# Optimization experiments

Hardware: AMD Instinct MI355X
Metric: run time of the kernel (lower is better)

## Reference

```python
import jax, jax.numpy as jnp
import numpy as np

EPS = 1e-6   # param.eps
DT = 1e-2    # param.dt
DX = 1.0     # param.dx
DY = 1.0     # param.dy
N_PARAM = 1.0  # param.N


def _lap(c, dx=1.0, dy=1.0):
    # 5-point periodic Laplacian stencil on the last two dims
    return ((jnp.roll(c, 1, -1) + jnp.roll(c, -1, -1) - 2.0 * c) / (dx * dx)
            + (jnp.roll(c, 1, -2) + jnp.roll(c, -1, -2) - 2.0 * c) / (dy * dy))


def _log_with_mask(m, eps=EPS):
    # masked positions get constant eps -> zero gradient there, like torch masked_fill
    return jnp.log(jnp.where(m < eps, eps, m))


def setup_inputs() -> dict:
    key = jax.random.key(0)
    ks = jax.random.split(key, 12)
    B, H, W = 8, 1024, 1024
    inp = {
        "cv": jax.random.uniform(ks[0], (B, H, W), dtype=jnp.float32),
        "ci": jax.random.uniform(ks[1], (B, H, W), dtype=jnp.float32),
        "eta": jax.random.uniform(ks[2], (B, H, W), dtype=jnp.float32),
    }
    names = ["energy_v0", "energy_i0", "kBT0", "kappa_v0", "kappa_i0",
             "kappa_eta0", "diff_v0", "diff_i0", "L0"]
    for i, n in enumerate(names):
        inp[n] = jax.random.uniform(ks[3 + i], (1,), dtype=jnp.float32)
    return inp


def reference(cv, ci, eta, energy_v0, energy_i0, kBT0, kappa_v0, kappa_i0,
              kappa_eta0, diff_v0, diff_i0, L0):
    energy_v = jnp.abs(energy_v0) + 0.001
    energy_i = jnp.abs(energy_i0) + 0.001
    kBT = jnp.abs(kBT0) + 0.001
    kappa_v = jnp.abs(kappa_v0) + 0.001
    kappa_i = jnp.abs(kappa_i0) + 0.001
    kappa_eta = jnp.abs(kappa_eta0) + 0.001
    diff_v = jnp.abs(diff_v0) + 0.001
    diff_i = jnp.abs(diff_i0) + 0.001
    L = jnp.abs(L0) + 0.001

    lap_cv = _lap(cv, DX, DY)
    lap_ci = _lap(ci, DX, DY)
    lap_eta = _lap(eta, DX, DY)

    h = (eta - 1.0) ** 2
    j = eta ** 2
    cs = 1.0 - cv - ci
    log_cv = _log_with_mask(cv)
    log_ci = _log_with_mask(ci)
    log_cs = _log_with_mask(cs)

    fs = energy_v * cv + energy_i * ci + kBT * (cv * log_cv + ci * log_ci + cs * log_cs)
    dfs_dcv = energy_v + kBT * (log_cv - log_cs)
    dfs_dci = energy_i + kBT * (log_ci - log_cs)

    fv = (cv - 1.0) ** 2 + ci ** 2
    dfv_dcv = 2.0 * (cv - 1.0)
    dfv_dci = 2.0 * ci

    dF_dcv = h * dfs_dcv + j * dfv_dcv - kappa_v * lap_cv
    dF_dci = h * dfs_dci + j * dfv_dci - kappa_i * lap_ci
    dF_deta = N_PARAM * (fs * 2.0 * (eta - 1.0) + fv * 2.0 * eta - kappa_eta * lap_eta)

    mv = diff_v * cv / kBT
    mi = diff_i * ci / kBT

    cv_new = jnp.clip(cv + DT * (mv * _lap(dF_dcv)), 0.0, 1.0)
    ci_new = jnp.clip(ci + DT * (mi * _lap(dF_dci)), 0.0, 1.0)
    eta_new = jnp.clip(eta + DT * (-L * dF_deta), 0.0, 1.0)
    return cv_new, ci_new, eta_new
```

## Files before the change

kernel.cpp:

```cpp
#include <hip/hip_runtime.h>

#define WMASK 1023
#define LOG2W 10
#define HW (1024 * 1024)

#define EPS 1e-6f
#define DT 1e-2f

#define TX 64
#define TY 16

#define RCH 18
#define RST 72
#define SST 64

typedef float f4 __attribute__((ext_vector_type(4)));

__device__ __forceinline__ float scal(const float* __restrict__ p) {
    return fabsf(p[0]) + 0.001f;
}
__device__ __forceinline__ float clip01(float v) {
    return fminf(fmaxf(v, 0.0f), 1.0f);
}
__device__ __forceinline__ float lg2m(float m) {
    return __log2f(fmaxf(m, EPS));
}

__global__ __launch_bounds__(256, 6) void irr_fused(
    const float* __restrict__ cv,
    const float* __restrict__ ci,
    const float* __restrict__ eta,
    const float* __restrict__ p_ev,
    const float* __restrict__ p_ei,
    const float* __restrict__ p_kbt,
    const float* __restrict__ p_kv,
    const float* __restrict__ p_ki,
    const float* __restrict__ p_ke,
    const float* __restrict__ p_dv,
    const float* __restrict__ p_di,
    const float* __restrict__ p_L,
    float* __restrict__ cv_new,
    float* __restrict__ ci_new,
    float* __restrict__ eta_new)
{
    __shared__ __attribute__((aligned(16))) float scv[20][RST];
    __shared__ __attribute__((aligned(16))) float sci[20][RST];
    __shared__ __attribute__((aligned(16))) float seta[18][RST];
    __shared__ __attribute__((aligned(16))) float sdv[16][SST];
    __shared__ __attribute__((aligned(16))) float sdi[16][SST];

    const int tid = threadIdx.x;
    const int x0 = blockIdx.x * TX;
    const int y0 = blockIdx.y * TY;
    const int bbase = blockIdx.z * HW;

    const float energy_v = scal(p_ev);
    const float energy_i = scal(p_ei);
    const float kBT      = scal(p_kbt);
    const float kappa_v  = scal(p_kv);
    const float kappa_i  = scal(p_ki);
    const float kappa_e  = scal(p_ke);
    const float diff_v   = scal(p_dv);
    const float diff_i   = scal(p_di);
    const float L        = scal(p_L);
    const float kl   = kBT * 0.69314718056f;
    const float dtl  = DT * L;
    const float dtrv = DT * diff_v / kBT;
    const float dtri = DT * diff_i / kBT;

    for (int t = tid; t < 1044; t += 256) {
        const float* __restrict__ src;
        float (*dstA)[RST];
        int r, gy0;
        if (t < 360)      { src = cv;  r = t;       gy0 = y0 - 2; dstA = scv; }
        else if (t < 720) { src = ci;  r = t - 360; gy0 = y0 - 2; dstA = sci; }
        else              { src = eta; r = t - 720; gy0 = y0 - 1; dstA = seta; }
        const int cx = r % RCH;
        const int cy = r / RCH;
        const int gx = (x0 - 4 + (cx << 2)) & WMASK;
        const int gy = (gy0 + cy) & WMASK;
        const f4 v = *(const f4*)(src + bbase + (gy << LOG2W) + gx);
        *(f4*)&dstA[cy][cx << 2] = v;
    }
    __syncthreads();

    const int k  = tid & 15;
    const int ey = tid >> 4;
    const int rx = (k << 2) + 4;

    const f4    cC = *(const f4*)&scv[ey + 2][rx];
    const f4    cU = *(const f4*)&scv[ey + 1][rx];
    const f4    cD = *(const f4*)&scv[ey + 3][rx];
    const float cL = scv[ey + 2][rx - 1];
    const float cR = scv[ey + 2][rx + 4];

    const f4    iC = *(const f4*)&sci[ey + 2][rx];
    const f4    iU = *(const f4*)&sci[ey + 1][rx];
    const f4    iD = *(const f4*)&sci[ey + 3][rx];
    const float iL = sci[ey + 2][rx - 1];
    const float iR = sci[ey + 2][rx + 4];

    const f4    eC = *(const f4*)&seta[ey + 1][rx];
    const f4    eU = *(const f4*)&seta[ey][rx];
    const f4    eD = *(const f4*)&seta[ey + 2][rx];
    const float eL = seta[ey + 1][rx - 1];
    const float eR = seta[ey + 1][rx + 4];

    f4 dv, di, en;
    #pragma unroll
    for (int j = 0; j < 4; ++j) {
        const float c0 = cC[j];
        const float i0 = iC[j];
        const float e0 = eC[j];
        const float cl = (j == 0) ? cL : cC[j - 1];
        const float cr = (j == 3) ? cR : cC[j + 1];
        const float il = (j == 0) ? iL : iC[j - 1];
        const float ir = (j == 3) ? iR : iC[j + 1];
        const float el = (j == 0) ? eL : eC[j - 1];
        const float er = (j == 3) ? eR : eC[j + 1];

        const float lap_cv  = cl + cr + cU[j] + cD[j] - 4.0f * c0;
        const float lap_ci  = il + ir + iU[j] + iD[j] - 4.0f * i0;
        const float lap_eta = el + er + eU[j] + eD[j] - 4.0f * e0;

        const float h  = (e0 - 1.0f) * (e0 - 1.0f);
        const float jj = e0 * e0;
        const float cs = 1.0f - c0 - i0;
        const float lgv = lg2m(c0);
        const float lgi = lg2m(i0);
        const float lgs = lg2m(cs);

        dv[j] = h * (energy_v + kl * (lgv - lgs)) + jj * (2.0f * (c0 - 1.0f))
              - kappa_v * lap_cv;
        di[j] = h * (energy_i + kl * (lgi - lgs)) + jj * (2.0f * i0)
              - kappa_i * lap_ci;

        const float fs = energy_v * c0 + energy_i * i0
                       + kl * (c0 * lgv + i0 * lgi + cs * lgs);
        const float fv = (c0 - 1.0f) * (c0 - 1.0f) + i0 * i0;
        const float dF_deta = fs * 2.0f * (e0 - 1.0f) + fv * 2.0f * e0
                            - kappa_e * lap_eta;
        en[j] = clip01(fmaf(-dtl, dF_deta, e0));
    }

    const int c = k << 2;
    *(f4*)&sdv[ey][c] = dv;
    *(f4*)&sdi[ey][c] = di;

    const int gidx = bbase + ((y0 + ey) << LOG2W) + (x0 + c);
    __builtin_nontemporal_store(en, (f4*)(eta_new + gidx));

    __syncthreads();

    auto evalpt = [&](int cr, int cc, int er) -> float2 {
        const float c0 = scv[cr][cc];
        const float lap_cv = scv[cr][cc - 1] + scv[cr][cc + 1]
                           + scv[cr - 1][cc] + scv[cr + 1][cc] - 4.0f * c0;
        const float i0 = sci[cr][cc];
        const float lap_ci = sci[cr][cc - 1] + sci[cr][cc + 1]
                           + sci[cr - 1][cc] + sci[cr + 1][cc] - 4.0f * i0;
        const float e0 = seta[er][cc];
        const float h  = (e0 - 1.0f) * (e0 - 1.0f);
        const float jj = e0 * e0;
        const float cs = 1.0f - c0 - i0;
        const float lgv = lg2m(c0);
        const float lgi = lg2m(i0);
        const float lgs = lg2m(cs);
        const float dvx = h * (energy_v + kl * (lgv - lgs))
                        + jj * (2.0f * (c0 - 1.0f)) - kappa_v * lap_cv;
        const float dix = h * (energy_i + kl * (lgi - lgs))
                        + jj * (2.0f * i0) - kappa_i * lap_ci;
        return make_float2(dvx, dix);
    };

    float vL, wL, vR, wR;
    if (k == 0) {
        const float2 r = evalpt(ey + 2, 3, ey + 1);
        vL = r.x; wL = r.y;
    } else {
        vL = sdv[ey][c - 1]; wL = sdi[ey][c - 1];
    }
    if (k == 15) {
        const float2 r = evalpt(ey + 2, 68, ey + 1);
        vR = r.x; wR = r.y;
    } else {
        vR = sdv[ey][c + 4]; wR = sdi[ey][c + 4];
    }

    f4 vU, wU, vD, wD;
    if (ey == 0) {
        #pragma unroll
        for (int j = 0; j < 4; ++j) {
            const float2 r = evalpt(1, rx + j, 0);
            vU[j] = r.x; wU[j] = r.y;
        }
    } else {
        vU = *(const f4*)&sdv[ey - 1][c];
        wU = *(const f4*)&sdi[ey - 1][c];
    }
    if (ey == 15) {
        #pragma unroll
        for (int j = 0; j < 4; ++j) {
            const float2 r = evalpt(18, rx + j, 17);
            vD[j] = r.x; wD[j] = r.y;
        }
    } else {
        vD = *(const f4*)&sdv[ey + 1][c];
        wD = *(const f4*)&sdi[ey + 1][c];
    }

    f4 outv, outi;
    #pragma unroll
    for (int j = 0; j < 4; ++j) {
        const float lv = ((j == 0) ? vL : dv[j - 1]) + ((j == 3) ? vR : dv[j + 1])
                       + vU[j] + vD[j] - 4.0f * dv[j];
        const float li = ((j == 0) ? wL : di[j - 1]) + ((j == 3) ? wR : di[j + 1])
                       + wU[j] + wD[j] - 4.0f * di[j];
        outv[j] = clip01(fmaf(dtrv * cC[j], lv, cC[j]));
        outi[j] = clip01(fmaf(dtri * iC[j], li, iC[j]));
    }
    __builtin_nontemporal_store(outv, (f4*)(cv_new + gidx));
    __builtin_nontemporal_store(outi, (f4*)(ci_new + gidx));
}

extern "C" void kernel_launch(void* const* d_in, const int* in_sizes, int n_in,
                              void* d_out, int out_size, void* d_ws, size_t ws_size,
                              hipStream_t stream) {
    const float* cv  = (const float*)d_in[0];
    const float* ci  = (const float*)d_in[1];
    const float* eta = (const float*)d_in[2];
    const float* p_ev  = (const float*)d_in[3];
    const float* p_ei  = (const float*)d_in[4];
    const float* p_kbt = (const float*)d_in[5];
    const float* p_kv  = (const float*)d_in[6];
    const float* p_ki  = (const float*)d_in[7];
    const float* p_ke  = (const float*)d_in[8];
    const float* p_dv  = (const float*)d_in[9];
    const float* p_di  = (const float*)d_in[10];
    const float* p_L   = (const float*)d_in[11];

    const int N = in_sizes[0];

    float* out     = (float*)d_out;
    float* cv_new  = out;
    float* ci_new  = out + N;
    float* eta_new = out + 2 * N;

    const dim3 block(256);
    const dim3 grid(1024 / TX, 1024 / TY, N / HW);

    irr_fused<<<grid, block, 0, stream>>>(cv, ci, eta, p_ev, p_ei, p_kbt,
                                          p_kv, p_ki, p_ke, p_dv, p_di, p_L,
                                          cv_new, ci_new, eta_new);
}
```

Before: 212.4 us.

## Process four row tiles per block with register-staged prefetch of next tile

Each block now walks four consecutive 16-row tiles instead of one, shrinking the grid by four. While a tile is computed, the next tile's halo loads are already in flight into registers and are written to shared memory after the current tile finishes, so global latency overlaps with compute. Barriers use a raw waitcnt plus s_barrier. This raises register pressure because 20 floats per thread are held across the compute, and it gives fewer blocks to hide latency. Halo rows are still reloaded for every tile rather than reused.

Result: slower. 397.1 us (+87.0%).

```diff
diff --git a/kernel.cpp b/kernel.cpp
--- a/kernel.cpp
+++ b/kernel.cpp
@@ -9,12 +9,15 @@
 
 #define TX 64
 #define TY 16
-
-#define RCH 18
+#define TPB 4
+
 #define RST 72
+#define NTASK 1044
 #define SST 64
 
 typedef float f4 __attribute__((ext_vector_type(4)));
+
+struct Stage { f4 v0, v1, v2, v3, v4; };
 
 __device__ __forceinline__ float scal(const float* __restrict__ p) {
     return fabsf(p[0]) + 0.001f;
@@ -24,6 +27,27 @@
 }
 __device__ __forceinline__ float lg2m(float m) {
     return __log2f(fmaxf(m, EPS));
+}
+
+__device__ __forceinline__ void lgkm_barrier() {
+    asm volatile("s_waitcnt lgkmcnt(0)" ::: "memory");
+    __builtin_amdgcn_s_barrier();
+}
+
+__device__ __forceinline__ f4 ld_task(int t, int x0, int y0t, int bbase,
+                                      const float* __restrict__ cv,
+                                      const float* __restrict__ ci,
+                                      const float* __restrict__ eta) {
+    const float* __restrict__ src;
+    int r, gy0;
+    if (t < 360)      { src = cv;  r = t;       gy0 = y0t - 2; }
+    else if (t < 720) { src = ci;  r = t - 360; gy0 = y0t - 2; }
+    else              { src = eta; r = t - 720; gy0 = y0t - 1; }
+    const int cx = r % 18;
+    const int cy = r / 18;
+    const int gx = (x0 - 4 + (cx << 2)) & WMASK;
+    const int gy = (gy0 + cy) & WMASK;
+    return *(const f4*)(src + bbase + (gy << LOG2W) + gx);
 }
 
 __global__ __launch_bounds__(256, 6) void irr_fused(
@@ -43,15 +67,17 @@
     float* __restrict__ ci_new,
     float* __restrict__ eta_new)
 {
-    __shared__ __attribute__((aligned(16))) float scv[20][RST];
-    __shared__ __attribute__((aligned(16))) float sci[20][RST];
-    __shared__ __attribute__((aligned(16))) float seta[18][RST];
+    __shared__ __attribute__((aligned(16))) float sraw[NTASK * 4];
     __shared__ __attribute__((aligned(16))) float sdv[16][SST];
     __shared__ __attribute__((aligned(16))) float sdi[16][SST];
 
+    float (*scv)[RST]  = (float(*)[RST])(sraw);
+    float (*sci)[RST]  = (float(*)[RST])(sraw + 1440);
+    float (*seta)[RST] = (float(*)[RST])(sraw + 2880);
+
     const int tid = threadIdx.x;
     const int x0 = blockIdx.x * TX;
-    const int y0 = blockIdx.y * TY;
+    const int y0 = blockIdx.y * (TY * TPB);
     const int bbase = blockIdx.z * HW;
 
     const float energy_v = scal(p_ev);
@@ -68,159 +94,177 @@
     const float dtrv = DT * diff_v / kBT;
     const float dtri = DT * diff_i / kBT;
 
-    for (int t = tid; t < 1044; t += 256) {
-        const float* __restrict__ src;
-        float (*dstA)[RST];
-        int r, gy0;
-        if (t < 360)      { src = cv;  r = t;       gy0 = y0 - 2; dstA = scv; }
-        else if (t < 720) { src = ci;  r = t - 360; gy0 = y0 - 2; dstA = sci; }
-        else              { src = eta; r = t - 720; gy0 = y0 - 1; dstA = seta; }
-        const int cx = r % RCH;
-        const int cy = r / RCH;
-        const int gx = (x0 - 4 + (cx << 2)) & WMASK;
-        const int gy = (gy0 + cy) & WMASK;
-        const f4 v = *(const f4*)(src + bbase + (gy << LOG2W) + gx);
-        *(f4*)&dstA[cy][cx << 2] = v;
-    }
-    __syncthreads();
+    auto load_tile = [&](int y0t) -> Stage {
+        Stage s;
+        s.v0 = ld_task(tid,       x0, y0t, bbase, cv, ci, eta);
+        s.v1 = ld_task(tid + 256, x0, y0t, bbase, cv, ci, eta);
+        s.v2 = ld_task(tid + 512, x0, y0t, bbase, cv, ci, eta);
+        s.v3 = ld_task(tid + 768, x0, y0t, bbase, cv, ci, eta);
+        if (tid < NTASK - 1024)
+            s.v4 = ld_task(tid + 1024, x0, y0t, bbase, cv, ci, eta);
+        return s;
+    };
+    auto store_stage = [&](const Stage& s) {
+        f4* dst = (f4*)sraw;
+        dst[tid]       = s.v0;
+        dst[tid + 256] = s.v1;
+        dst[tid + 512] = s.v2;
+        dst[tid + 768] = s.v3;
+        if (tid < NTASK - 1024) dst[tid + 1024] = s.v4;
+    };
+
+    Stage rg = load_tile(y0);
+    store_stage(rg);
+    rg = load_tile(y0 + TY);
+    lgkm_barrier();
 
     const int k  = tid & 15;
     const int ey = tid >> 4;
     const int rx = (k << 2) + 4;
-
-    const f4    cC = *(const f4*)&scv[ey + 2][rx];
-    const f4    cU = *(const f4*)&scv[ey + 1][rx];
-    const f4    cD = *(const f4*)&scv[ey + 3][rx];
-    const float cL = scv[ey + 2][rx - 1];
-    const float cR = scv[ey + 2][rx + 4];
-
-    const f4    iC = *(const f4*)&sci[ey + 2][rx];
-    const f4    iU = *(const f4*)&sci[ey + 1][rx];
-    const f4    iD = *(const f4*)&sci[ey + 3][rx];
-    const float iL = sci[ey + 2][rx - 1];
-    const float iR = sci[ey + 2][rx + 4];
-
-    const f4    eC = *(const f4*)&seta[ey + 1][rx];
-    const f4    eU = *(const f4*)&seta[ey][rx];
-    const f4    eD = *(const f4*)&seta[ey + 2][rx];
-    const float eL = seta[ey + 1][rx - 1];
-    const float eR = seta[ey + 1][rx + 4];
-
-    f4 dv, di, en;
-    #pragma unroll
-    for (int j = 0; j < 4; ++j) {
-        const float c0 = cC[j];
-        const float i0 = iC[j];
-        const float e0 = eC[j];
-        const float cl = (j == 0) ? cL : cC[j - 1];
-        const float cr = (j == 3) ? cR : cC[j + 1];
-        const float il = (j == 0) ? iL : iC[j - 1];
-        const float ir = (j == 3) ? iR : iC[j + 1];
-        const float el = (j == 0) ? eL : eC[j - 1];
-        const float er = (j == 3) ? eR : eC[j + 1];
-
-        const float lap_cv  = cl + cr + cU[j] + cD[j] - 4.0f * c0;
-        const float lap_ci  = il + ir + iU[j] + iD[j] - 4.0f * i0;
-        const float lap_eta = el + er + eU[j] + eD[j] - 4.0f * e0;
-
-        const float h  = (e0 - 1.0f) * (e0 - 1.0f);
-        const float jj = e0 * e0;
-        const float cs = 1.0f - c0 - i0;
-        const float lgv = lg2m(c0);
-        const float lgi = lg2m(i0);
-        const float lgs = lg2m(cs);
-
-        dv[j] = h * (energy_v + kl * (lgv - lgs)) + jj * (2.0f * (c0 - 1.0f))
-              - kappa_v * lap_cv;
-        di[j] = h * (energy_i + kl * (lgi - lgs)) + jj * (2.0f * i0)
-              - kappa_i * lap_ci;
-
-        const float fs = energy_v * c0 + energy_i * i0
-                       + kl * (c0 * lgv + i0 * lgi + cs * lgs);
-        const float fv = (c0 - 1.0f) * (c0 - 1.0f) + i0 * i0;
-        const float dF_deta = fs * 2.0f * (e0 - 1.0f) + fv * 2.0f * e0
-                            - kappa_e * lap_eta;
-        en[j] = clip01(fmaf(-dtl, dF_deta, e0));
-    }
-
-    const int c = k << 2;
-    *(f4*)&sdv[ey][c] = dv;
-    *(f4*)&sdi[ey][c] = di;
-
-    const int gidx = bbase + ((y0 + ey) << LOG2W) + (x0 + c);
-    __builtin_nontemporal_store(en, (f4*)(eta_new + gidx));
-
-    __syncthreads();
-
-    auto evalpt = [&](int cr, int cc, int er) -> float2 {
-        const float c0 = scv[cr][cc];
-        const float lap_cv = scv[cr][cc - 1] + scv[cr][cc + 1]
-                           + scv[cr - 1][cc] + scv[cr + 1][cc] - 4.0f * c0;
-        const float i0 = sci[cr][cc];
-        const float lap_ci = sci[cr][cc - 1] + sci[cr][cc + 1]
-                           + sci[cr - 1][cc] + sci[cr + 1][cc] - 4.0f * i0;
-        const float e0 = seta[er][cc];
-        const float h  = (e0 - 1.0f) * (e0 - 1.0f);
-        const float jj = e0 * e0;
-        const float cs = 1.0f - c0 - i0;
-        const float lgv = lg2m(c0);
-        const float lgi = lg2m(i0);
-        const float lgs = lg2m(cs);
-        const float dvx = h * (energy_v + kl * (lgv - lgs))
-                        + jj * (2.0f * (c0 - 1.0f)) - kappa_v * lap_cv;
-        const float dix = h * (energy_i + kl * (lgi - lgs))
-                        + jj * (2.0f * i0) - kappa_i * lap_ci;
-        return make_float2(dvx, dix);
-    };
-
-    float vL, wL, vR, wR;
-    if (k == 0) {
-        const float2 r = evalpt(ey + 2, 3, ey + 1);
-        vL = r.x; wL = r.y;
-    } else {
-        vL = sdv[ey][c - 1]; wL = sdi[ey][c - 1];
-    }
-    if (k == 15) {
-        const float2 r = evalpt(ey + 2, 68, ey + 1);
-        vR = r.x; wR = r.y;
-    } else {
-        vR = sdv[ey][c + 4]; wR = sdi[ey][c + 4];
-    }
-
-    f4 vU, wU, vD, wD;
-    if (ey == 0) {
+    const int c  = k << 2;
+
+    for (int tl = 0; tl < TPB; ++tl) {
+        const int y0t = y0 + tl * TY;
+
+        const f4    cC = *(const f4*)&scv[ey + 2][rx];
+        const f4    cU = *(const f4*)&scv[ey + 1][rx];
+        const f4    cD = *(const f4*)&scv[ey + 3][rx];
+        const float cL = scv[ey + 2][rx - 1];
+        const float cR = scv[ey + 2][rx + 4];
+
+        const f4    iC = *(const f4*)&sci[ey + 2][rx];
+        const f4    iU = *(const f4*)&sci[ey + 1][rx];
+        const f4    iD = *(const f4*)&sci[ey + 3][rx];
+        const float iL = sci[ey + 2][rx - 1];
+        const float iR = sci[ey + 2][rx + 4];
+
+        const f4    eC = *(const f4*)&seta[ey + 1][rx];
+        const f4    eU = *(const f4*)&seta[ey][rx];
+        const f4    eD = *(const f4*)&seta[ey + 2][rx];
+        const float eL = seta[ey + 1][rx - 1];
+        const float eR = seta[ey + 1][rx + 4];
+
+        f4 dv, di, en;
         #pragma unroll
         for (int j = 0; j < 4; ++j) {
-            const float2 r = evalpt(1, rx + j, 0);
-            vU[j] = r.x; wU[j] = r.y;
-        }
-    } else {
-        vU = *(const f4*)&sdv[ey - 1][c];
-        wU = *(const f4*)&sdi[ey - 1][c];
-    }
-    if (ey == 15) {
+            const float c0 = cC[j];
+            const float i0 = iC[j];
+            const float e0 = eC[j];
+            const float cl = (j == 0) ? cL : cC[j - 1];
+            const float cr = (j == 3) ? cR : cC[j + 1];
+            const float il = (j == 0) ? iL : iC[j - 1];
+            const float ir = (j == 3) ? iR : iC[j + 1];
+            const float el = (j == 0) ? eL : eC[j - 1];
+            const float er = (j == 3) ? eR : eC[j + 1];
+
+            const float lap_cv  = cl + cr + cU[j] + cD[j] - 4.0f * c0;
+            const float lap_ci  = il + ir + iU[j] + iD[j] - 4.0f * i0;
+            const float lap_eta = el + er + eU[j] + eD[j] - 4.0f * e0;
+
+            const float h  = (e0 - 1.0f) * (e0 - 1.0f);
+            const float jj = e0 * e0;
+            const float cs = 1.0f - c0 - i0;
+            const float lgv = lg2m(c0);
+            const float lgi = lg2m(i0);
+            const float lgs = lg2m(cs);
+
+            dv[j] = h * (energy_v + kl * (lgv - lgs)) + jj * (2.0f * (c0 - 1.0f))
+                  - kappa_v * lap_cv;
+            di[j] = h * (energy_i + kl * (lgi - lgs)) + jj * (2.0f * i0)
+                  - kappa_i * lap_ci;
+
+            const float fs = energy_v * c0 + energy_i * i0
+                           + kl * (c0 * lgv + i0 * lgi + cs * lgs);
+            const float fv = (c0 - 1.0f) * (c0 - 1.0f) + i0 * i0;
+            const float dF_deta = fs * 2.0f * (e0 - 1.0f) + fv * 2.0f * e0
+                                - kappa_e * lap_eta;
+            en[j] = clip01(fmaf(-dtl, dF_deta, e0));
+        }
+
+        *(f4*)&sdv[ey][c] = dv;
+        *(f4*)&sdi[ey][c] = di;
+
+        lgkm_barrier();
+
+        auto evalpt = [&](int cr, int cc, int er) -> float2 {
+            const float c0 = scv[cr][cc];
+            const float lap_cv = scv[cr][cc - 1] + scv[cr][cc + 1]
+                               + scv[cr - 1][cc] + scv[cr + 1][cc] - 4.0f * c0;
+            const float i0 = sci[cr][cc];
+            const float lap_ci = sci[cr][cc - 1] + sci[cr][cc + 1]
+                               + sci[cr - 1][cc] + sci[cr + 1][cc] - 4.0f * i0;
+            const float e0 = seta[er][cc];
+            const float h  = (e0 - 1.0f) * (e0 - 1.0f);
+            const float jj = e0 * e0;
+            const float cs = 1.0f - c0 - i0;
+            const float lgv = lg2m(c0);
+            const float lgi = lg2m(i0);
+            const float lgs = lg2m(cs);
+            const float dvx = h * (energy_v + kl * (lgv - lgs))
+                            + jj * (2.0f * (c0 - 1.0f)) - kappa_v * lap_cv;
+            const float dix = h * (energy_i + kl * (lgi - lgs))
+                            + jj * (2.0f * i0) - kappa_i * lap_ci;
+            return make_float2(dvx, dix);
+        };
+
+        float vL, wL, vR, wR;
+        if (k == 0) {
+            const float2 r = evalpt(ey + 2, 3, ey + 1);
+            vL = r.x; wL = r.y;
+        } else {
+            vL = sdv[ey][c - 1]; wL = sdi[ey][c - 1];
+        }
+        if (k == 15) {
+            const float2 r = evalpt(ey + 2, 68, ey + 1);
+            vR = r.x; wR = r.y;
+        } else {
+            vR = sdv[ey][c + 4]; wR = sdi[ey][c + 4];
+        }
+
+        f4 vU, wU, vD, wD;
+        if (ey == 0) {
+            #pragma unroll
+            for (int j = 0; j < 4; ++j) {
+                const float2 r = evalpt(1, rx + j, 0);
+                vU[j] = r.x; wU[j] = r.y;
+            }
+        } else {
+            vU = *(const f4*)&sdv[ey - 1][c];
+            wU = *(const f4*)&sdi[ey - 1][c];
+        }
+        if (ey == 15) {
+            #pragma unroll
+            for (int j = 0; j < 4; ++j) {
+                const float2 r = evalpt(18, rx + j, 17);
+                vD[j] = r.x; wD[j] = r.y;
+            }
+        } else {
+            vD = *(const f4*)&sdv[ey + 1][c];
+            wD = *(const f4*)&sdi[ey + 1][c];
+        }
+
+        const int gidx = bbase + ((y0t + ey) << LOG2W) + (x0 + c);
+        f4 outv, outi;
         #pragma unroll
         for (int j = 0; j < 4; ++j) {
-            const float2 r = evalpt(18, rx + j, 17);
-            vD[j] = r.x; wD[j] = r.y;
-        }
-    } else {
-        vD = *(const f4*)&sdv[ey + 1][c];
-        wD = *(const f4*)&sdi[ey + 1][c];
+            const float lv = ((j == 0) ? vL : dv[j - 1]) + ((j == 3) ? vR : dv[j + 1])
+                           + vU[j] + vD[j] - 4.0f * dv[j];
+            const float li = ((j == 0) ? wL : di[j - 1]) + ((j == 3) ? wR : di[j + 1])
+                           + wU[j] + wD[j] - 4.0f * di[j];
+            outv[j] = clip01(fmaf(dtrv * cC[j], lv, cC[j]));
+            outi[j] = clip01(fmaf(dtri * iC[j], li, iC[j]));
+        }
+        __builtin_nontemporal_store(en,   (f4*)(eta_new + gidx));
+        __builtin_nontemporal_store(outv, (f4*)(cv_new + gidx));
+        __builtin_nontemporal_store(outi, (f4*)(ci_new + gidx));
+
+        if (tl + 1 < TPB) {
+            lgkm_barrier();
+            store_stage(rg);
+            if (tl + 2 < TPB) rg = load_tile(y0 + (tl + 2) * TY);
+            lgkm_barrier();
+        }
     }
-
-    f4 outv, outi;
-    #pragma unroll
-    for (int j = 0; j < 4; ++j) {
-        const float lv = ((j == 0) ? vL : dv[j - 1]) + ((j == 3) ? vR : dv[j + 1])
-                       + vU[j] + vD[j] - 4.0f * dv[j];
-        const float li = ((j == 0) ? wL : di[j - 1]) + ((j == 3) ? wR : di[j + 1])
-                       + wU[j] + wD[j] - 4.0f * di[j];
-        outv[j] = clip01(fmaf(dtrv * cC[j], lv, cC[j]));
-        outi[j] = clip01(fmaf(dtri * iC[j], li, iC[j]));
-    }
-    __builtin_nontemporal_store(outv, (f4*)(cv_new + gidx));
-    __builtin_nontemporal_store(outi, (f4*)(ci_new + gidx));
 }
 
 extern "C" void kernel_launch(void* const* d_in, const int* in_sizes, int n_in,
@@ -247,7 +291,7 @@
     float* eta_new = out + 2 * N;
 
     const dim3 block(256);
-    const dim3 grid(1024 / TX, 1024 / TY, N / HW);
+    const dim3 grid(1024 / TX, 1024 / (TY * TPB), N / HW);
 
     irr_fused<<<grid, block, 0, stream>>>(cv, ci, eta, p_ev, p_ei, p_kbt,
                                           p_kv, p_ki, p_ke, p_dv, p_di, p_L,
```
